# Optimization experiments

Hardware: AMD Instinct MI355X
Metric: run time of the kernel (lower is better)

## Reference

```python
import jax, jax.numpy as jnp
import numpy as np

EPS = 1e-5


def _lin(k, fan_in, fan_out):
    return jax.random.normal(k, (fan_in, fan_out), jnp.float32) / np.sqrt(fan_in)


def setup_inputs() -> dict:
    key = jax.random.key(0)
    ks = jax.random.split(key, 12)
    N, E, F_in, H, G, S = 50000, 800000, 128, 64, 256, 64
    x = jax.random.normal(ks[0], (N, F_in), jnp.float32)
    edge_index = jax.random.randint(ks[1], (2, E), 0, N, dtype=jnp.int32)
    batch = jnp.sort(jax.random.randint(ks[2], (N,), 0, G, dtype=jnp.int32))
    sigma = jax.random.normal(ks[3], (G, S), jnp.float32)
    return {
        "x": x, "edge_index": edge_index, "batch": batch, "sigma": sigma,
        # GCN layers
        "W1": _lin(ks[4], F_in, H), "b1": jnp.zeros(H, jnp.float32),
        "g1": jnp.ones(H, jnp.float32), "be1": jnp.zeros(H, jnp.float32),
        "W2": _lin(ks[5], H, H), "b2": jnp.zeros(H, jnp.float32),
        "g2": jnp.ones(H, jnp.float32), "be2": jnp.zeros(H, jnp.float32),
        "W3": _lin(ks[6], H, H), "b3": jnp.zeros(H, jnp.float32),
        "g3": jnp.ones(H, jnp.float32), "be3": jnp.zeros(H, jnp.float32),
        # feed-forward branch
        "Wf1": _lin(ks[7], S, 2 * H), "bf1": jnp.zeros(2 * H, jnp.float32),
        "Wf2": _lin(ks[8], 2 * H, H), "bf2": jnp.zeros(H, jnp.float32),
        # fusion head
        "Wfu": _lin(ks[9], 2 * H, 1), "bfu": jnp.zeros(1, jnp.float32),
    }


def _gcn(x, W, b, src, dst, dis, N):
    """PyG GCNConv: D^-1/2 (A+I) D^-1/2 X W + b, with self-loops."""
    h = x @ W                                        # [N, H]
    norm = (dis[src] * dis[dst])[:, None]            # [E, 1]
    agg = jax.ops.segment_sum(h[src] * norm, dst, num_segments=N)
    agg = agg + h * (dis * dis)[:, None]             # self-loop contribution
    return agg + b


def _bn(x, g, be):
    mu = x.mean(axis=0)
    var = x.var(axis=0)  # biased, matches torch BN normalization
    return (x - mu) * jax.lax.rsqrt(var + EPS) * g + be


def reference(x, edge_index, batch, sigma,
              W1, b1, g1, be1, W2, b2, g2, be2, W3, b3, g3, be3,
              Wf1, bf1, Wf2, bf2, Wfu, bfu):
    N = x.shape[0]
    G = sigma.shape[0]
    src, dst = edge_index[0], edge_index[1]
    # symmetric normalization with self-loops: deg = 1 + in-degree
    deg = jax.ops.segment_sum(jnp.ones(src.shape[0], x.dtype), dst, num_segments=N) + 1.0
    dis = jax.lax.rsqrt(deg)

    h = jax.nn.relu(_bn(_gcn(x, W1, b1, src, dst, dis, N), g1, be1))
    h_res = h
    h = jax.nn.relu(_bn(_gcn(h, W2, b2, src, dst, dis, N), g2, be2) + h_res)
    h = jax.nn.relu(_bn(_gcn(h, W3, b3, src, dst, dis, N), g3, be3))

    # global mean pool over graphs
    sums = jax.ops.segment_sum(h, batch, num_segments=G)
    cnt = jax.ops.segment_sum(jnp.ones(N, x.dtype), batch, num_segments=G)
    gcn_emb = sums / jnp.maximum(cnt, 1.0)[:, None]   # [G, H]

    # feed-forward branch (dropout off in eval)
    f = jax.nn.relu(sigma @ Wf1 + bf1)
    f = jax.nn.relu(f @ Wf2 + bf2)                    # [G, H]

    fused = jnp.concatenate([gcn_emb, f], axis=1)     # [G, 2H]
    out = fused @ Wfu + bfu
    return out.squeeze(-1)                            # [G]
```

## Files before the change

kernel.cpp:

```cpp
#include <hip/hip_runtime.h>
#include <hip/hip_bf16.h>

typedef float f32x4 __attribute__((ext_vector_type(4)));

__device__ __forceinline__ float b2f(unsigned short u) {
    union { unsigned int i; float f; } t; t.i = ((unsigned int)u) << 16; return t.f;
}

__global__ void k_hist(const int* __restrict__ dst, int* __restrict__ cnt, int E) {
    int e = blockIdx.x * blockDim.x + threadIdx.x;
    if (e < E) atomicAdd(&cnt[dst[e]], 1);
}

__global__ void k_scanA(const int* __restrict__ cnt, int* __restrict__ bsum, int N) {
    __shared__ int sh[256];
    int i = blockIdx.x * 256 + threadIdx.x;
    sh[threadIdx.x] = (i < N) ? cnt[i] : 0;
    __syncthreads();
    for (int off = 128; off > 0; off >>= 1) {
        if (threadIdx.x < off) sh[threadIdx.x] += sh[threadIdx.x + off];
        __syncthreads();
    }
    if (threadIdx.x == 0) bsum[blockIdx.x] = sh[0];
}

__global__ void k_scanB(int* __restrict__ bsum, int nb) {
    __shared__ int sh[1024];
    int t = threadIdx.x;
    sh[t] = (t < nb) ? bsum[t] : 0;
    __syncthreads();
    for (int off = 1; off < 1024; off <<= 1) {
        int v = (t >= off) ? sh[t - off] : 0;
        __syncthreads();
        sh[t] += v;
        __syncthreads();
    }
    if (t < nb) bsum[t] = (t == 0) ? 0 : sh[t - 1];
}

__global__ void k_scanC(const int* __restrict__ cnt, const int* __restrict__ boff,
                        int* __restrict__ row_ptr, int4* __restrict__ rc4,
                        float* __restrict__ dis, int N) {
    __shared__ int sh[256];
    int i = blockIdx.x * 256 + threadIdx.x;
    int v = (i < N) ? cnt[i] : 0;
    sh[threadIdx.x] = v;
    __syncthreads();
    for (int off = 1; off < 256; off <<= 1) {
        int u = (threadIdx.x >= off) ? sh[threadIdx.x - off] : 0;
        __syncthreads();
        sh[threadIdx.x] += u;
        __syncthreads();
    }
    if (i < N) {
        int start = sh[threadIdx.x] - v + boff[blockIdx.x];
        float d = rsqrtf((float)v + 1.0f);
        row_ptr[i] = start;
        rc4[i] = make_int4(start, v, __float_as_int(d), 0);
        dis[i] = d;
    }
}

__global__ void k_fill(const int* __restrict__ src, const int* __restrict__ dst,
                       const int* __restrict__ row_ptr, int* __restrict__ cursor,
                       int* __restrict__ csr_src, int E) {
    int e = blockIdx.x * blockDim.x + threadIdx.x;
    if (e < E) {
        int d = dst[e];
        int pos = row_ptr[d] + atomicAdd(&cursor[d], 1);
        csr_src[pos] = src[e];
    }
}

template <int K, int MODE>
__global__ void __launch_bounds__(256, 2) k_gemm_lds(const float* __restrict__ in,
                                                     const float* __restrict__ in2,
                                                     const float* __restrict__ W,
                                                     const float* __restrict__ dis,
                                                     const float* __restrict__ statsB,
                                                     const float* __restrict__ gB,
                                                     const float* __restrict__ beB,
                                                     const float* __restrict__ statsA,
                                                     const float* __restrict__ gA,
                                                     const float* __restrict__ beA,
                                                     __hip_bfloat16* __restrict__ out,
                                                     float invN, int N) {
    constexpr int KF = K / 4;
    __shared__ float Wl[K * 64];
    __shared__ float4 xt[32 * KF];
    __shared__ float dl[32];
    __shared__ float scb[64], shb[64], sca[64], sha[64];
    for (int i = threadIdx.x; i < K * 16; i += 256)
        ((float4*)Wl)[i] = ((const float4*)W)[i];
    if constexpr (MODE >= 1) {
        if (threadIdx.x < 64) {
            int c = threadIdx.x;
            float mu  = statsB[c] * invN;
            float var = statsB[64 + c] * invN - mu * mu;
            float s   = gB[c] * rsqrtf(var + 1e-5f);
            scb[c] = s; shb[c] = beB[c] - mu * s;
        }
    }
    if constexpr (MODE == 2) {
        if (threadIdx.x >= 64 && threadIdx.x < 128) {
            int c = threadIdx.x - 64;
            float mu  = statsA[c] * invN;
            float var = statsA[64 + c] * invN - mu * mu;
            float s   = gA[c] * rsqrtf(var + 1e-5f);
            sca[c] = s; sha[c] = beA[c] - mu * s;
        }
    }
    int col = threadIdx.x & 63;
    int rg  = threadIdx.x >> 6;
    const float4* in4  = (const float4*)in;
    const float4* in24 = (const float4*)in2;
    const float4 zero4 = {0.f, 0.f, 0.f, 0.f};
    int ntiles = (N + 31) >> 5;
    for (int t = blockIdx.x; t < ntiles; t += gridDim.x) {
        int base = t * 32;
        __syncthreads();
        for (int i = threadIdx.x; i < 32 * KF; i += 256) {
            int r = i / KF, f = i - r * KF;
            int row = base + r;
            float4 v = zero4;
            if (row < N) {
                v = in4[(size_t)row * KF + f];
                if constexpr (MODE >= 1) {
                    float4 sc = ((const float4*)scb)[f];
                    float4 sh = ((const float4*)shb)[f];
                    float rx = 0.f, ry = 0.f, rz = 0.f, rw = 0.f;
                    if constexpr (MODE == 2) {
                        float4 u  = in24[(size_t)row * KF + f];
                        float4 sa = ((const float4*)sca)[f];
                        float4 ha = ((const float4*)sha)[f];
                        rx = fmaxf(u.x * sa.x + ha.x, 0.f);
                        ry = fmaxf(u.y * sa.y + ha.y, 0.f);
                        rz = fmaxf(u.z * sa.z + ha.z, 0.f);
                        rw = fmaxf(u.w * sa.w + ha.w, 0.f);
                    }
                    v.x = fmaxf(v.x * sc.x + sh.x + rx, 0.f);
                    v.y = fmaxf(v.y * sc.y + sh.y + ry, 0.f);
                    v.z = fmaxf(v.z * sc.z + sh.z + rz, 0.f);
                    v.w = fmaxf(v.w * sc.w + sh.w + rw, 0.f);
                }
            }
            xt[i] = v;
        }
        if (threadIdx.x < 32) {
            int row = base + threadIdx.x;
            dl[threadIdx.x] = (row < N) ? dis[row] : 0.f;
        }
        __syncthreads();
        float acc[8] = {0.f, 0.f, 0.f, 0.f, 0.f, 0.f, 0.f, 0.f};
#pragma unroll 2
        for (int kg = 0; kg < KF; ++kg) {
            float w0 = Wl[(4 * kg + 0) * 64 + col];
            float w1 = Wl[(4 * kg + 1) * 64 + col];
            float w2 = Wl[(4 * kg + 2) * 64 + col];
            float w3 = Wl[(4 * kg + 3) * 64 + col];
#pragma unroll
            for (int i = 0; i < 8; ++i) {
                float4 xv = xt[(rg * 8 + i) * KF + kg];
                acc[i] = fmaf(xv.w, w3, fmaf(xv.z, w2, fmaf(xv.y, w1, fmaf(xv.x, w0, acc[i]))));
            }
        }
        int r0 = base + rg * 8;
        if (r0 + 7 < N) {
#pragma unroll
            for (int i = 0; i < 8; ++i)
                out[(size_t)(r0 + i) * 64 + col] = __float2bfloat16(acc[i] * dl[rg * 8 + i]);
        } else {
#pragma unroll
            for (int i = 0; i < 8; ++i)
                if (r0 + i < N)
                    out[(size_t)(r0 + i) * 64 + col] = __float2bfloat16(acc[i] * dl[rg * 8 + i]);
        }
    }
}

__global__ void __launch_bounds__(256) k_gather8v2(const int4* __restrict__ rc4,
                                                   const int* __restrict__ csr_src,
                                                   const __hip_bfloat16* __restrict__ hs,
                                                   const float* __restrict__ b,
                                                   float* __restrict__ z,
                                                   float* __restrict__ stats, int N) {
    const unsigned short* hsu = (const unsigned short*)hs;
    int tid  = threadIdx.x;
    int lane = tid & 63;
    int w    = tid >> 6;
    int grp  = lane >> 3;
    int sub  = lane & 7;
    float vb[8];
    *(float4*)&vb[0] = *(const float4*)(b + sub * 8);
    *(float4*)&vb[4] = *(const float4*)(b + sub * 8 + 4);
    float ps[8] = {0,0,0,0,0,0,0,0}, pq[8] = {0,0,0,0,0,0,0,0};
    int wid = blockIdx.x * 4 + w;
    int nw  = gridDim.x * 4;
    const float4 zero4 = {0.f, 0.f, 0.f, 0.f};
    for (int base = wid * 2; base < N; base += nw * 2) {
        int nA = base;
        int nB = base + 1;
        bool hasB = (nB < N);
        int4 ra = rc4[nA];
        int4 rb = hasB ? rc4[nB] : make_int4(0, 0, 0, 0);
        int startA = ra.x, cA = ra.y; float dA = __int_as_float(ra.z);
        int startB = rb.x, cB = rb.y; float dB = __int_as_float(rb.z);
        int sA0 = -1, sA1 = -1, sA2 = -1, sB0 = -1, sB1 = -1, sB2 = -1;
        if (grp      < cA) sA0 = __builtin_nontemporal_load(&csr_src[startA + grp]);
        if (8 + grp  < cA) sA1 = __builtin_nontemporal_load(&csr_src[startA + 8 + grp]);
        if (16 + grp < cA) sA2 = __builtin_nontemporal_load(&csr_src[startA + 16 + grp]);
        if (grp      < cB) sB0 = __builtin_nontemporal_load(&csr_src[startB + grp]);
        if (8 + grp  < cB) sB1 = __builtin_nontemporal_load(&csr_src[startB + 8 + grp]);
        if (16 + grp < cB) sB2 = __builtin_nontemporal_load(&csr_src[startB + 16 + grp]);
        float4 rA0 = zero4, rA1 = zero4, rA2 = zero4;
        float4 rB0 = zero4, rB1 = zero4, rB2 = zero4;
        if (sA0 >= 0) rA0 = *(const float4*)(hsu + (size_t)sA0 * 64 + sub * 8);
        if (sA1 >= 0) rA1 = *(const float4*)(hsu + (size_t)sA1 * 64 + sub * 8);
        if (sA2 >= 0) rA2 = *(const float4*)(hsu + (size_t)sA2 * 64 + sub * 8);
        if (sB0 >= 0) rB0 = *(const float4*)(hsu + (size_t)sB0 * 64 + sub * 8);
        if (sB1 >= 0) rB1 = *(const float4*)(hsu + (size_t)sB1 * 64 + sub * 8);
        if (sB2 >= 0) rB2 = *(const float4*)(hsu + (size_t)sB2 * 64 + sub * 8);
        float4 selfA = *(const float4*)(hsu + (size_t)nA * 64 + sub * 8);
        float4 selfB = hasB ? *(const float4*)(hsu + (size_t)nB * 64 + sub * 8) : zero4;
        float accA[8], accB[8];
        {
            const unsigned short* uA0 = (const unsigned short*)&rA0;
            const unsigned short* uA1 = (const unsigned short*)&rA1;
            const unsigned short* uA2 = (const unsigned short*)&rA2;
            const unsigned short* uB0 = (const unsigned short*)&rB0;
            const unsigned short* uB1 = (const unsigned short*)&rB1;
            const unsigned short* uB2 = (const unsigned short*)&rB2;
#pragma unroll
            for (int i = 0; i < 8; ++i) {
                accA[i] = b2f(uA0[i]) + b2f(uA1[i]) + b2f(uA2[i]);
                accB[i] = b2f(uB0[i]) + b2f(uB1[i]) + b2f(uB2[i]);
            }
        }
        for (int j = 24; j + grp < cA; j += 8) {
            int s = csr_src[startA + j + grp];
            float4 raw = *(const float4*)(hsu + (size_t)s * 64 + sub * 8);
            const unsigned short* us = (const unsigned short*)&raw;
#pragma unroll
            for (int i = 0; i < 8; ++i) accA[i] += b2f(us[i]);
        }
        for (int j = 24; j + grp < cB; j += 8) {
            int s = csr_src[startB + j + grp];
            float4 raw = *(const float4*)(hsu + (size_t)s * 64 + sub * 8);
            const unsigned short* us = (const unsigned short*)&raw;
#pragma unroll
            for (int i = 0; i < 8; ++i) accB[i] += b2f(us[i]);
        }
#pragma unroll
        for (int i = 0; i < 8; ++i) { accA[i] += __shfl_xor(accA[i], 8);  accB[i] += __shfl_xor(accB[i], 8); }
#pragma unroll
        for (int i = 0; i < 8; ++i) { accA[i] += __shfl_xor(accA[i], 16); accB[i] += __shfl_xor(accB[i], 16); }
#pragma unroll
        for (int i = 0; i < 8; ++i) { accA[i] += __shfl_xor(accA[i], 32); accB[i] += __shfl_xor(accB[i], 32); }
        if (grp == 0) {
            const unsigned short* suA = (const unsigned short*)&selfA;
            float v[8];
#pragma unroll
            for (int i = 0; i < 8; ++i) {
                v[i] = (accA[i] + b2f(suA[i])) * dA + vb[i];
                ps[i] += v[i];
                pq[i] += v[i] * v[i];
            }
            __builtin_nontemporal_store(*(f32x4*)&v[0], (f32x4*)(z + (size_t)nA * 64 + sub * 8));
            __builtin_nontemporal_store(*(f32x4*)&v[4], (f32x4*)(z + (size_t)nA * 64 + sub * 8 + 4));
            if (hasB) {
                const unsigned short* suB = (const unsigned short*)&selfB;
#pragma unroll
                for (int i = 0; i < 8; ++i) {
                    v[i] = (accB[i] + b2f(suB[i])) * dB + vb[i];
                    ps[i] += v[i];
                    pq[i] += v[i] * v[i];
                }
                __builtin_nontemporal_store(*(f32x4*)&v[0], (f32x4*)(z + (size_t)nB * 64 + sub * 8));
                __builtin_nontemporal_store(*(f32x4*)&v[4], (f32x4*)(z + (size_t)nB * 64 + sub * 8 + 4));
            }
        }
    }
    __shared__ float ssum[4][64], ssq[4][64];
    if (grp == 0) {
        *(float4*)&ssum[w][sub * 8]     = *(float4*)&ps[0];
        *(float4*)&ssum[w][sub * 8 + 4] = *(float4*)&ps[4];
        *(float4*)&ssq[w][sub * 8]      = *(float4*)&pq[0];
        *(float4*)&ssq[w][sub * 8 + 4]  = *(float4*)&pq[4];
    }
    __syncthreads();
    if (tid < 64) {
        float s = ssum[0][tid] + ssum[1][tid] + ssum[2][tid] + ssum[3][tid];
        float q = ssq[0][tid] + ssq[1][tid] + ssq[2][tid] + ssq[3][tid];
        atomicAdd(&stats[tid], s);
        atomicAdd(&stats[64 + tid], q);
    }
}

__global__ void k_norm_pool(const float* __restrict__ z, const float* __restrict__ stats,
                            const float* __restrict__ g, const float* __restrict__ be,
                            const int* __restrict__ batch, float* __restrict__ psums,
                            float* __restrict__ pcnt, float invN, int N, int per) {
    int lane = threadIdx.x & 63;
    int wave = (blockIdx.x * blockDim.x + threadIdx.x) >> 6;
    int begin = wave * per;
    if (begin >= N) return;
    int end = begin + per; if (end > N) end = N;
    float mu  = stats[lane] * invN;
    float var = stats[64 + lane] * invN - mu * mu;
    float sc  = g[lane] * rsqrtf(var + 1e-5f);
    float sh  = be[lane] - mu * sc;
    int   cur = batch[begin];
    float run = 0.f;
    int   crun = 0;
    for (int n = begin; n < end; ++n) {
        int gg = batch[n];
        if (gg != cur) {
            atomicAdd(&psums[(size_t)cur * 64 + lane], run);
            if (lane == 0) atomicAdd(&pcnt[cur], (float)crun);
            run = 0.f; crun = 0; cur = gg;
        }
        float v = fmaxf(z[(size_t)n * 64 + lane] * sc + sh, 0.f);
        run += v; crun++;
    }
    atomicAdd(&psums[(size_t)cur * 64 + lane], run);
    if (lane == 0) atomicAdd(&pcnt[cur], (float)crun);
}

__global__ void k_head(const float* __restrict__ sigma, const float* __restrict__ Wf1,
                       const float* __restrict__ bf1, const float* __restrict__ Wf2,
                       const float* __restrict__ bf2, const float* __restrict__ Wfu,
                       const float* __restrict__ bfu, const float* __restrict__ sums,
                       const float* __restrict__ cnt, float* __restrict__ out) {
    int g = blockIdx.x;
    int t = threadIdx.x;
    __shared__ float srow[64], f1[128], f2[64];
    if (t < 64) srow[t] = sigma[(size_t)g * 64 + t];
    __syncthreads();
    {
        float acc = bf1[t];
        for (int s = 0; s < 64; ++s) acc += srow[s] * Wf1[s * 128 + t];
        f1[t] = fmaxf(acc, 0.f);
    }
    __syncthreads();
    if (t < 64) {
        float a2 = bf2[t];
        for (int k = 0; k < 128; ++k) a2 += f1[k] * Wf2[k * 64 + t];
        f2[t] = fmaxf(a2, 0.f);
    }
    __syncthreads();
    if (t < 64) {
        float inv    = 1.0f / fmaxf(cnt[g], 1.0f);
        float pooled = sums[(size_t)g * 64 + t] * inv;
        float contrib = pooled * Wfu[t] + f2[t] * Wfu[64 + t];
#pragma unroll
        for (int o = 32; o > 0; o >>= 1) contrib += __shfl_down(contrib, o);
        if (t == 0) out[g] = contrib + bfu[0];
    }
}

extern "C" void kernel_launch(void* const* d_in, const int* in_sizes, int n_in,
                              void* d_out, int out_size, void* d_ws, size_t ws_size,
                              hipStream_t stream) {
    const float* x     = (const float*)d_in[0];
    const int*   ei    = (const int*)d_in[1];
    const int*   batch = (const int*)d_in[2];
    const float* sigma = (const float*)d_in[3];
    const float* W1 = (const float*)d_in[4];  const float* b1 = (const float*)d_in[5];
    const float* g1 = (const float*)d_in[6];  const float* be1 = (const float*)d_in[7];
    const float* W2 = (const float*)d_in[8];  const float* b2 = (const float*)d_in[9];
    const float* g2 = (const float*)d_in[10]; const float* be2 = (const float*)d_in[11];
    const float* W3 = (const float*)d_in[12]; const float* b3 = (const float*)d_in[13];
    const float* g3 = (const float*)d_in[14]; const float* be3 = (const float*)d_in[15];
    const float* Wf1 = (const float*)d_in[16]; const float* bf1 = (const float*)d_in[17];
    const float* Wf2 = (const float*)d_in[18]; const float* bf2 = (const float*)d_in[19];
    const float* Wfu = (const float*)d_in[20]; const float* bfu = (const float*)d_in[21];

    const int N = in_sizes[0] / 128;
    const int E = in_sizes[1] / 2;
    const int G = in_sizes[3] / 64;
    const int* src = ei;
    const int* dst = ei + E;

    float* ws   = (float*)d_ws;
    float* bufA = ws;
    float* bufB = bufA + (size_t)N * 64;
    float* bufC = bufB + (size_t)N * 64;
    __hip_bfloat16* hsb = (__hip_bfloat16*)(bufC + (size_t)N * 64);
    float* dis  = (float*)(hsb + (size_t)N * 64);
    int4*  rc4     = (int4*)(dis + N);
    int*   row_ptr = (int*)(rc4 + N);
    int*   bsum    = row_ptr + N;
    int*   csr_src = bsum + 1024;
    int*   cnt     = csr_src + E;
    int*   cursor  = cnt + N;
    float* stats1  = (float*)(cursor + N);
    float* stats2  = stats1 + 128;
    float* stats3  = stats2 + 128;
    float* psums   = stats3 + 128;
    float* pcnt    = psums + (size_t)G * 64;
    size_t zero_bytes = ((char*)(pcnt + G)) - ((char*)cnt);

    const float invN = 1.0f / (float)N;
    const int nb     = (N + 255) / 256;

    hipMemsetAsync(cnt, 0, zero_bytes, stream);

    k_hist<<<(E + 255) / 256, 256, 0, stream>>>(dst, cnt, E);
    k_scanA<<<nb, 256, 0, stream>>>(cnt, bsum, N);
    k_scanB<<<1, 1024, 0, stream>>>(bsum, nb);
    k_scanC<<<nb, 256, 0, stream>>>(cnt, bsum, row_ptr, rc4, dis, N);
    k_fill<<<(E + 255) / 256, 256, 0, stream>>>(src, dst, row_ptr, cursor, csr_src, E);

    k_gemm_lds<128, 0><<<1024, 256, 0, stream>>>(x, nullptr, W1, dis,
        nullptr, nullptr, nullptr, nullptr, nullptr, nullptr, hsb, invN, N);
    k_gather8v2<<<2048, 256, 0, stream>>>(rc4, csr_src, hsb, b1, bufB, stats1, N);

    k_gemm_lds<64, 1><<<1024, 256, 0, stream>>>(bufB, nullptr, W2, dis,
        stats1, g1, be1, nullptr, nullptr, nullptr, hsb, invN, N);
    k_gather8v2<<<2048, 256, 0, stream>>>(rc4, csr_src, hsb, b2, bufA, stats2, N);

    k_gemm_lds<64, 2><<<1024, 256, 0, stream>>>(bufA, bufB, W3, dis,
        stats2, g2, be2, stats1, g1, be1, hsb, invN, N);
    k_gather8v2<<<2048, 256, 0, stream>>>(rc4, csr_src, hsb, b3, bufC, stats3, N);

    {
        const int waves = 8192;
        int per = (N + waves - 1) / waves;
        k_norm_pool<<<2048, 256, 0, stream>>>(bufC, stats3, g3, be3, batch, psums, pcnt, invN, N, per);
    }

    k_head<<<G, 128, 0, stream>>>(sigma, Wf1, bf1, Wf2, bf2, Wfu, bfu, psums, pcnt, (float*)d_out);
}
```

Baseline: 377.2 us.

## Split bf16 feature table into column halves and gather each half separately

The GEMM now writes its bf16 output as two separate 32-column tables instead of one 64-column table. The gather runs as two launches, one per half, each reading 64-byte rows with 16 neighbours in flight per wave instead of 8. The aim is to shrink the table each gather pass touches so it fits better in cache, which should raise hit rates on the random neighbour reads. In exchange it doubles the gather launches and re-reads the CSR indices and row info, adds one more shuffle-reduction stage, and makes each z store only half a row.

Result: slower. 436.2 us (+15.7%).

```diff
diff --git a/kernel.cpp b/kernel.cpp
--- a/kernel.cpp
+++ b/kernel.cpp
@@ -5,6 +5,10 @@
 
 __device__ __forceinline__ float b2f(unsigned short u) {
     union { unsigned int i; float f; } t; t.i = ((unsigned int)u) << 16; return t.f;
+}
+__device__ __forceinline__ unsigned short f2b(float f) {
+    __hip_bfloat16 h = __float2bfloat16(f);
+    return *reinterpret_cast<unsigned short*>(&h);
 }
 
 __global__ void k_hist(const int* __restrict__ dst, int* __restrict__ cnt, int E) {
@@ -83,7 +87,8 @@
                                                      const float* __restrict__ statsA,
                                                      const float* __restrict__ gA,
                                                      const float* __restrict__ beA,
-                                                     __hip_bfloat16* __restrict__ out,
+                                                     unsigned short* __restrict__ tabl,
+                                                     unsigned short* __restrict__ tabh,
                                                      float invN, int N) {
     constexpr int KF = K / 4;
     __shared__ float Wl[K * 64];
@@ -112,6 +117,8 @@
     }
     int col = threadIdx.x & 63;
     int rg  = threadIdx.x >> 6;
+    unsigned short* tab = (col < 32) ? tabl : tabh;
+    int cc = col & 31;
     const float4* in4  = (const float4*)in;
     const float4* in24 = (const float4*)in2;
     const float4 zero4 = {0.f, 0.f, 0.f, 0.f};
@@ -168,88 +175,82 @@
         if (r0 + 7 < N) {
 #pragma unroll
             for (int i = 0; i < 8; ++i)
-                out[(size_t)(r0 + i) * 64 + col] = __float2bfloat16(acc[i] * dl[rg * 8 + i]);
+                tab[(size_t)(r0 + i) * 32 + cc] = f2b(acc[i] * dl[rg * 8 + i]);
         } else {
 #pragma unroll
             for (int i = 0; i < 8; ++i)
                 if (r0 + i < N)
-                    out[(size_t)(r0 + i) * 64 + col] = __float2bfloat16(acc[i] * dl[rg * 8 + i]);
-        }
-    }
-}
-
-__global__ void __launch_bounds__(256) k_gather8v2(const int4* __restrict__ rc4,
-                                                   const int* __restrict__ csr_src,
-                                                   const __hip_bfloat16* __restrict__ hs,
-                                                   const float* __restrict__ b,
-                                                   float* __restrict__ z,
-                                                   float* __restrict__ stats, int N) {
-    const unsigned short* hsu = (const unsigned short*)hs;
+                    tab[(size_t)(r0 + i) * 32 + cc] = f2b(acc[i] * dl[rg * 8 + i]);
+        }
+    }
+}
+
+template <int HALF>
+__global__ void __launch_bounds__(256) k_gath32(const int4* __restrict__ rc4,
+                                                const int* __restrict__ csr_src,
+                                                const unsigned short* __restrict__ tab,
+                                                const float* __restrict__ b,
+                                                float* __restrict__ z,
+                                                float* __restrict__ stats, int N) {
     int tid  = threadIdx.x;
     int lane = tid & 63;
     int w    = tid >> 6;
-    int grp  = lane >> 3;
-    int sub  = lane & 7;
+    int grp  = lane >> 2;
+    int sub  = lane & 3;
     float vb[8];
-    *(float4*)&vb[0] = *(const float4*)(b + sub * 8);
-    *(float4*)&vb[4] = *(const float4*)(b + sub * 8 + 4);
+    *(float4*)&vb[0] = *(const float4*)(b + HALF * 32 + sub * 8);
+    *(float4*)&vb[4] = *(const float4*)(b + HALF * 32 + sub * 8 + 4);
     float ps[8] = {0,0,0,0,0,0,0,0}, pq[8] = {0,0,0,0,0,0,0,0};
     int wid = blockIdx.x * 4 + w;
     int nw  = gridDim.x * 4;
     const float4 zero4 = {0.f, 0.f, 0.f, 0.f};
     for (int base = wid * 2; base < N; base += nw * 2) {
-        int nA = base;
-        int nB = base + 1;
+        int nA = base, nB = base + 1;
         bool hasB = (nB < N);
         int4 ra = rc4[nA];
         int4 rb = hasB ? rc4[nB] : make_int4(0, 0, 0, 0);
         int startA = ra.x, cA = ra.y; float dA = __int_as_float(ra.z);
         int startB = rb.x, cB = rb.y; float dB = __int_as_float(rb.z);
-        int sA0 = -1, sA1 = -1, sA2 = -1, sB0 = -1, sB1 = -1, sB2 = -1;
-        if (grp      < cA) sA0 = __builtin_nontemporal_load(&csr_src[startA + grp]);
-        if (8 + grp  < cA) sA1 = __builtin_nontemporal_load(&csr_src[startA + 8 + grp]);
-        if (16 + grp < cA) sA2 = __builtin_nontemporal_load(&csr_src[startA + 16 + grp]);
-        if (grp      < cB) sB0 = __builtin_nontemporal_load(&csr_src[startB + grp]);
-        if (8 + grp  < cB) sB1 = __builtin_nontemporal_load(&csr_src[startB + 8 + grp]);
-        if (16 + grp < cB) sB2 = __builtin_nontemporal_load(&csr_src[startB + 16 + grp]);
-        float4 rA0 = zero4, rA1 = zero4, rA2 = zero4;
-        float4 rB0 = zero4, rB1 = zero4, rB2 = zero4;
-        if (sA0 >= 0) rA0 = *(const float4*)(hsu + (size_t)sA0 * 64 + sub * 8);
-        if (sA1 >= 0) rA1 = *(const float4*)(hsu + (size_t)sA1 * 64 + sub * 8);
-        if (sA2 >= 0) rA2 = *(const float4*)(hsu + (size_t)sA2 * 64 + sub * 8);
-        if (sB0 >= 0) rB0 = *(const float4*)(hsu + (size_t)sB0 * 64 + sub * 8);
-        if (sB1 >= 0) rB1 = *(const float4*)(hsu + (size_t)sB1 * 64 + sub * 8);
-        if (sB2 >= 0) rB2 = *(const float4*)(hsu + (size_t)sB2 * 64 + sub * 8);
-        float4 selfA = *(const float4*)(hsu + (size_t)nA * 64 + sub * 8);
-        float4 selfB = hasB ? *(const float4*)(hsu + (size_t)nB * 64 + sub * 8) : zero4;
+        int sA0 = -1, sA1 = -1, sB0 = -1, sB1 = -1;
+        if (grp < cA)      sA0 = __builtin_nontemporal_load(&csr_src[startA + grp]);
+        if (16 + grp < cA) sA1 = __builtin_nontemporal_load(&csr_src[startA + 16 + grp]);
+        if (grp < cB)      sB0 = __builtin_nontemporal_load(&csr_src[startB + grp]);
+        if (16 + grp < cB) sB1 = __builtin_nontemporal_load(&csr_src[startB + 16 + grp]);
+        float4 rA0 = zero4, rA1 = zero4, rB0 = zero4, rB1 = zero4;
+        if (sA0 >= 0) rA0 = *(const float4*)(tab + (size_t)sA0 * 32 + sub * 8);
+        if (sA1 >= 0) rA1 = *(const float4*)(tab + (size_t)sA1 * 32 + sub * 8);
+        if (sB0 >= 0) rB0 = *(const float4*)(tab + (size_t)sB0 * 32 + sub * 8);
+        if (sB1 >= 0) rB1 = *(const float4*)(tab + (size_t)sB1 * 32 + sub * 8);
+        float4 selfA = (grp == 0) ? *(const float4*)(tab + (size_t)nA * 32 + sub * 8) : zero4;
+        float4 selfB = (hasB && grp == 0) ? *(const float4*)(tab + (size_t)nB * 32 + sub * 8) : zero4;
         float accA[8], accB[8];
         {
             const unsigned short* uA0 = (const unsigned short*)&rA0;
             const unsigned short* uA1 = (const unsigned short*)&rA1;
-            const unsigned short* uA2 = (const unsigned short*)&rA2;
             const unsigned short* uB0 = (const unsigned short*)&rB0;
             const unsigned short* uB1 = (const unsigned short*)&rB1;
-            const unsigned short* uB2 = (const unsigned short*)&rB2;
 #pragma unroll
             for (int i = 0; i < 8; ++i) {
-                accA[i] = b2f(uA0[i]) + b2f(uA1[i]) + b2f(uA2[i]);
-                accB[i] = b2f(uB0[i]) + b2f(uB1[i]) + b2f(uB2[i]);
+                accA[i] = b2f(uA0[i]) + b2f(uA1[i]);
+                accB[i] = b2f(uB0[i]) + b2f(uB1[i]);
             }
         }
-        for (int j = 24; j + grp < cA; j += 8) {
+        for (int j = 32; j + grp < cA; j += 16) {
             int s = csr_src[startA + j + grp];
-            float4 raw = *(const float4*)(hsu + (size_t)s * 64 + sub * 8);
+            float4 raw = *(const float4*)(tab + (size_t)s * 32 + sub * 8);
             const unsigned short* us = (const unsigned short*)&raw;
 #pragma unroll
             for (int i = 0; i < 8; ++i) accA[i] += b2f(us[i]);
         }
-        for (int j = 24; j + grp < cB; j += 8) {
+        for (int j = 32; j + grp < cB; j += 16) {
             int s = csr_src[startB + j + grp];
-            float4 raw = *(const float4*)(hsu + (size_t)s * 64 + sub * 8);
+            float4 raw = *(const float4*)(tab + (size_t)s * 32 + sub * 8);
             const unsigned short* us = (const unsigned short*)&raw;
 #pragma unroll
             for (int i = 0; i < 8; ++i) accB[i] += b2f(us[i]);
         }
+#pragma unroll
+        for (int i = 0; i < 8; ++i) { accA[i] += __shfl_xor(accA[i], 4);  accB[i] += __shfl_xor(accB[i], 4); }
 #pragma unroll
         for (int i = 0; i < 8; ++i) { accA[i] += __shfl_xor(accA[i], 8);  accB[i] += __shfl_xor(accB[i], 8); }
 #pragma unroll
@@ -265,8 +266,8 @@
                 ps[i] += v[i];
                 pq[i] += v[i] * v[i];
             }
-            __builtin_nontemporal_store(*(f32x4*)&v[0], (f32x4*)(z + (size_t)nA * 64 + sub * 8));
-            __builtin_nontemporal_store(*(f32x4*)&v[4], (f32x4*)(z + (size_t)nA * 64 + sub * 8 + 4));
+            __builtin_nontemporal_store(*(f32x4*)&v[0], (f32x4*)(z + (size_t)nA * 64 + HALF * 32 + sub * 8));
+            __builtin_nontemporal_store(*(f32x4*)&v[4], (f32x4*)(z + (size_t)nA * 64 + HALF * 32 + sub * 8 + 4));
             if (hasB) {
                 const unsigned short* suB = (const unsigned short*)&selfB;
 #pragma unroll
@@ -275,12 +276,12 @@
                     ps[i] += v[i];
                     pq[i] += v[i] * v[i];
                 }
-                __builtin_nontemporal_store(*(f32x4*)&v[0], (f32x4*)(z + (size_t)nB * 64 + sub * 8));
-                __builtin_nontemporal_store(*(f32x4*)&v[4], (f32x4*)(z + (size_t)nB * 64 + sub * 8 + 4));
+                __builtin_nontemporal_store(*(f32x4*)&v[0], (f32x4*)(z + (size_t)nB * 64 + HALF * 32 + sub * 8));
+                __builtin_nontemporal_store(*(f32x4*)&v[4], (f32x4*)(z + (size_t)nB * 64 + HALF * 32 + sub * 8 + 4));
             }
         }
     }
-    __shared__ float ssum[4][64], ssq[4][64];
+    __shared__ float ssum[4][32], ssq[4][32];
     if (grp == 0) {
         *(float4*)&ssum[w][sub * 8]     = *(float4*)&ps[0];
         *(float4*)&ssum[w][sub * 8 + 4] = *(float4*)&ps[4];
@@ -288,11 +289,11 @@
         *(float4*)&ssq[w][sub * 8 + 4]  = *(float4*)&pq[4];
     }
     __syncthreads();
-    if (tid < 64) {
+    if (tid < 32) {
         float s = ssum[0][tid] + ssum[1][tid] + ssum[2][tid] + ssum[3][tid];
         float q = ssq[0][tid] + ssq[1][tid] + ssq[2][tid] + ssq[3][tid];
-        atomicAdd(&stats[tid], s);
-        atomicAdd(&stats[64 + tid], q);
+        atomicAdd(&stats[HALF * 32 + tid], s);
+        atomicAdd(&stats[64 + HALF * 32 + tid], q);
     }
 }
 
@@ -385,8 +386,9 @@
     float* bufA = ws;
     float* bufB = bufA + (size_t)N * 64;
     float* bufC = bufB + (size_t)N * 64;
-    __hip_bfloat16* hsb = (__hip_bfloat16*)(bufC + (size_t)N * 64);
-    float* dis  = (float*)(hsb + (size_t)N * 64);
+    unsigned short* tabl = (unsigned short*)(bufC + (size_t)N * 64);
+    unsigned short* tabh = tabl + (size_t)N * 32;
+    float* dis  = (float*)(tabh + (size_t)N * 32);
     int4*  rc4     = (int4*)(dis + N);
     int*   row_ptr = (int*)(rc4 + N);
     int*   bsum    = row_ptr + N;
@@ -412,16 +414,19 @@
     k_fill<<<(E + 255) / 256, 256, 0, stream>>>(src, dst, row_ptr, cursor, csr_src, E);
 
     k_gemm_lds<128, 0><<<1024, 256, 0, stream>>>(x, nullptr, W1, dis,
-        nullptr, nullptr, nullptr, nullptr, nullptr, nullptr, hsb, invN, N);
-    k_gather8v2<<<2048, 256, 0, stream>>>(rc4, csr_src, hsb, b1, bufB, stats1, N);
+        nullptr, nullptr, nullptr, nullptr, nullptr, nullptr, tabl, tabh, invN, N);
+    k_gath32<0><<<2048, 256, 0, stream>>>(rc4, csr_src, tabl, b1, bufB, stats1, N);
+    k_gath32<1><<<2048, 256, 0, stream>>>(rc4, csr_src, tabh, b1, bufB, stats1, N);
 
     k_gemm_lds<64, 1><<<1024, 256, 0, stream>>>(bufB, nullptr, W2, dis,
-        stats1, g1, be1, nullptr, nullptr, nullptr, hsb, invN, N);
-    k_gather8v2<<<2048, 256, 0, stream>>>(rc4, csr_src, hsb, b2, bufA, stats2, N);
+        stats1, g1, be1, nullptr, nullptr, nullptr, tabl, tabh, invN, N);
+    k_gath32<0><<<2048, 256, 0, stream>>>(rc4, csr_src, tabl, b2, bufA, stats2, N);
+    k_gath32<1><<<2048, 256, 0, stream>>>(rc4, csr_src, tabh, b2, bufA, stats2, N);
 
     k_gemm_lds<64, 2><<<1024, 256, 0, stream>>>(bufA, bufB, W3, dis,
-        stats2, g2, be2, stats1, g1, be1, hsb, invN, N);
-    k_gather8v2<<<2048, 256, 0, stream>>>(rc4, csr_src, hsb, b3, bufC, stats3, N);
+        stats2, g2, be2, stats1, g1, be1, tabl, tabh, invN, N);
+    k_gath32<0><<<2048, 256, 0, stream>>>(rc4, csr_src, tabl, b3, bufC, stats3, N);
+    k_gath32<1><<<2048, 256, 0, stream>>>(rc4, csr_src, tabh, b3, bufC, stats3, N);
 
     {
         const int waves = 8192;
```
